# Kernel optimization log

Hardware: AMD Instinct MI355X
Metric: run time of the kernel (lower is better)

The kernel has to match this reference:

```python
import jax, jax.numpy as jnp
import numpy as np

N_NODES = 50000
N_EDGES = 400000
C_NODE = 128
C_EDGE = 256
# PyG: round(c_in + (c_out-c_in)*f)
H1, H2, H3 = 166, 192, 218


def setup_inputs() -> dict:
    key = jax.random.key(0)
    ks = jax.random.split(key, 20)
    x = jax.random.normal(ks[0], (N_NODES, C_NODE), dtype=jnp.float32)
    edge_index = jax.random.randint(ks[1], (2, N_EDGES), 0, N_NODES, dtype=jnp.int64)

    def glorot(k, fan_in, fan_out):
        s = jnp.sqrt(6.0 / (fan_in + fan_out)).astype(jnp.float32)
        return jax.random.uniform(k, (fan_in, fan_out), jnp.float32, -s, s)

    dims_e = [(C_NODE, H1), (H1, H2), (H2, H3), (H3, C_EDGE)]
    dims_n = [(C_NODE, C_NODE)] * 4
    inp = {"x": x, "edge_index": edge_index}
    for i, (fi, fo) in enumerate(dims_e, 1):
        inp[f"W{i}e"] = glorot(ks[1 + i], fi, fo)
        inp[f"b{i}e"] = jnp.zeros((fo,), jnp.float32)
    for i, (fi, fo) in enumerate(dims_n, 1):
        inp[f"W{i}n"] = glorot(ks[9 + i], fi, fo)
        inp[f"b{i}n"] = jnp.zeros((fo,), jnp.float32)
    return inp


def _gcn_norm(edge_index, n_nodes):
    # add self loops, then symmetric normalization (PyG gcn_norm, improved=False)
    loops = jnp.arange(n_nodes, dtype=edge_index.dtype)
    src = jnp.concatenate([edge_index[0], loops])
    dst = jnp.concatenate([edge_index[1], loops])
    deg = jax.ops.segment_sum(jnp.ones_like(dst, dtype=jnp.float32), dst, num_segments=n_nodes)
    dinv = jnp.where(deg > 0, jax.lax.rsqrt(deg), 0.0)
    norm = dinv[src] * dinv[dst]  # [E+N]
    return src, dst, norm


def _gcn_conv(h_in, W, b, src, dst, norm, n_nodes):
    h = h_in @ W                      # [N, C_out] dense transform first (PyG order)
    msg = h[src] * norm[:, None]      # gather + scale, [E+N, C_out]
    agg = jax.ops.segment_sum(msg, dst, num_segments=n_nodes)
    return agg + b


def _forward(x, edge_index, We, be, Wn, bn):
    n = x.shape[0]
    src, dst, norm = _gcn_norm(edge_index, n)
    e = x
    for i in range(4):
        e = _gcn_conv(e, We[i], be[i], src, dst, norm, n)
        e = jax.nn.relu(e) if i < 3 else jax.nn.sigmoid(e)
    v = x
    for i in range(4):
        v = _gcn_conv(v, Wn[i], bn[i], src, dst, norm, n)
        v = jax.nn.relu(v) if i < 3 else jax.nn.sigmoid(v)
    return e, v


def reference(x, edge_index, W1e, b1e, W2e, b2e, W3e, b3e, W4e, b4e,
              W1n, b1n, W2n, b2n, W3n, b3n, W4n, b4n):
    We = [W1e, W2e, W3e, W4e]
    be = [b1e, b2e, b3e, b4e]
    Wn = [W1n, W2n, W3n, W4n]
    bn = [b1n, b2n, b3n, b4n]
    return _forward(x, edge_index, We, be, Wn, bn)
```

## Files before the change

kernel.cpp:

```cpp
#include <hip/hip_runtime.h>
#include <hip/hip_bf16.h>
#include <cstdint>
#include <cstddef>

typedef __hip_bfloat16 bf16;
typedef __attribute__((ext_vector_type(8))) short bf16x8;
typedef __attribute__((ext_vector_type(4))) float f32x4;

#define NN 50000
#define NE 400000

struct PTab {
    const void* p[17];
    int n[17];
};

__device__ __forceinline__ float bf2f(unsigned short u) {
    return __uint_as_float(((unsigned)u) << 16);
}
__device__ __forceinline__ unsigned short f2bf(float f) {
    __hip_bfloat16 h = __float2bfloat16(f);
    return *reinterpret_cast<unsigned short*>(&h);
}
__device__ __forceinline__ float fin(float v) {
    return (v == v && v > -1e30f && v < 1e30f) ? v : 0.0f;
}
__device__ __forceinline__ float rd(const void* p, int i, int f) {
    return f ? ((const float*)p)[i] : bf2f(((const unsigned short*)p)[i]);
}

__device__ __forceinline__ void gl16(const void* g, void* l) {
    __builtin_amdgcn_global_load_lds(
        (const __attribute__((address_space(1))) unsigned int*)g,
        (__attribute__((address_space(3))) unsigned int*)l, 16, 0, 0);
}

__global__ void k_probe(PTab tab, const int* __restrict__ ei, int* __restrict__ flags) {
    __shared__ int zc, bc, sAny;
    for (int t = 0; t < 17; ++t) {
        if (threadIdx.x == 0) { zc = 0; bc = 0; }
        __syncthreads();
        int words = tab.n[t] >> 1;
        if (words > 256) words = 256;
        if ((int)threadIdx.x < words) {
            unsigned w = ((const unsigned*)tab.p[t])[threadIdx.x];
            if (w == 0u) atomicAdd(&zc, 1);
            else {
                int e = (w >> 7) & 0xFF;
                if (e >= 100 && e <= 140) atomicAdd(&bc, 1);
            }
        }
        __syncthreads();
        if (threadIdx.x == 0) {
            int nz = words - zc;
            flags[t] = (nz == 0 || 2 * bc >= nz) ? 0 : 1;
        }
        __syncthreads();
    }
    if (threadIdx.x == 0) sAny = 0;
    __syncthreads();
    int any = 0;
    for (int i = threadIdx.x; i < 2048; i += 256) any |= ei[2 * i + 1];
    if (any) sAny = 1;
    __syncthreads();
    if (threadIdx.x == 0) flags[17] = sAny;
}

struct WSeg {
    const void* src[8];
    unsigned short* wh[8];
    unsigned short* wl[8];
    int f[8], K[8], M[8], Kp[8];
    int b0[9];
};

__global__ void k_wsplitall(WSeg G, const int* __restrict__ flags) {
    int bid = blockIdx.x;
    int seg = 0;
    #pragma unroll
    for (int t = 1; t < 8; ++t) if (bid >= G.b0[t]) seg = t;
    int n = bid - G.b0[seg];
    int k = threadIdx.x;
    int Kp = G.Kp[seg];
    if (k >= Kp) return;
    float v = 0.0f;
    if (k < G.K[seg] && n < G.M[seg])
        v = fin(rd(G.src[seg], k * G.M[seg] + n, flags[G.f[seg]]));
    unsigned short hi = f2bf(v);
    unsigned short lo = f2bf(v - bf2f(hi));
    G.wh[seg][(size_t)n * Kp + k] = hi;
    G.wl[seg][(size_t)n * Kp + k] = lo;
}

struct MOff { int m[8]; int mp[8]; };

__global__ void k_biasall(PTab tab, const int* __restrict__ flags, MOff mo,
                          float* __restrict__ dst) {
    int l = blockIdx.x;
    int fidx = 2 + 2 * l;
    int M = tab.n[fidx];
    int i = threadIdx.x;
    if (i < mo.mp[l])
        dst[mo.m[l] + i] = (i < M) ? fin(rd(tab.p[fidx], i, flags[fidx])) : 0.0f;
}

__global__ void k_repack(const int* __restrict__ ei, const int* __restrict__ flags,
                         int* __restrict__ src, int* __restrict__ dst,
                         int* __restrict__ deg) {
    int e = blockIdx.x * blockDim.x + threadIdx.x;
    if (e >= NE) return;
    int s, d;
    if (flags[17]) { s = ei[e]; d = ei[NE + e]; }
    else           { s = ei[2 * e]; d = ei[2 * (NE + e)]; }
    s = min(max(s, 0), NN - 1);
    d = min(max(d, 0), NN - 1);
    src[e] = s;
    dst[e] = d;
    atomicAdd(&deg[d], 1);
}

__global__ void k_scan1(const int* __restrict__ deg, int* __restrict__ rowp,
                        int* __restrict__ part) {
    __shared__ int s[512];
    int tid = threadIdx.x, i = blockIdx.x * 512 + tid;
    int v = (i < NN) ? deg[i] : 0;
    s[tid] = v;
    __syncthreads();
    for (int off = 1; off < 512; off <<= 1) {
        int t = (tid >= off) ? s[tid - off] : 0;
        __syncthreads();
        s[tid] += t;
        __syncthreads();
    }
    if (i < NN) rowp[i] = s[tid] - v;
    if (tid == 511) part[blockIdx.x] = s[511];
}
__global__ void k_scan2(int* __restrict__ part, int nb) {
    __shared__ int s[128];
    int tid = threadIdx.x;
    int v = (tid < nb) ? part[tid] : 0;
    s[tid] = v;
    __syncthreads();
    for (int off = 1; off < 128; off <<= 1) {
        int t = (tid >= off) ? s[tid - off] : 0;
        __syncthreads();
        s[tid] += t;
        __syncthreads();
    }
    if (tid < nb) part[tid] = s[tid] - v;
}
__global__ void k_scan3(int* __restrict__ rowp, const int* __restrict__ part,
                        const int* __restrict__ deg, float* __restrict__ dinv) {
    int i = blockIdx.x * blockDim.x + threadIdx.x;
    if (i < NN) {
        rowp[i] += part[i >> 9];
        dinv[i] = rsqrtf((float)deg[i] + 1.0f);
    }
    if (i == 0) rowp[NN] = NE;
}

__global__ void k_fill(const int* __restrict__ src, const int* __restrict__ dst,
                       const int* __restrict__ rowp, int* __restrict__ cursor,
                       int* __restrict__ colv) {
    int e = blockIdx.x * blockDim.x + threadIdx.x;
    if (e >= NE) return;
    int d = dst[e];
    int p = atomicAdd(&cursor[d], 1);
    colv[rowp[d] + p] = src[e];
}

__global__ void k_xin(const void* __restrict__ x, const int* __restrict__ flags,
                      const float* __restrict__ dinv, unsigned short* __restrict__ xs) {
    int t = blockIdx.x * blockDim.x + threadIdx.x;
    if (t >= NN * 16) return;
    int i = t >> 4, c = (t & 15) * 8;
    float d = dinv[i];
    int f = flags[0];
    const float* xf = (const float*)x + (size_t)i * 128 + c;
    const unsigned short* xb = (const unsigned short*)x + (size_t)i * 128 + c;
    unsigned short o[8];
    #pragma unroll
    for (int j = 0; j < 8; ++j)
        o[j] = f2bf(fin(f ? xf[j] : bf2f(xb[j])) * d);
    *(uint4*)(xs + (size_t)i * 128 + c) = *(uint4*)o;
}

__launch_bounds__(256)
__global__ void k_gather(const unsigned short* __restrict__ in, int istride,
                         unsigned short* __restrict__ out, int ostride, int lanes,
                         const int* __restrict__ rowp, const int* __restrict__ colv,
                         const float* __restrict__ dinv) {
    const int node = blockIdx.x * 4 + (threadIdx.x >> 6);
    if (node >= NN) return;
    const int lane = threadIdx.x & 63;
    const int beg = rowp[node], end = rowp[node + 1];
    float a[8] = {0.f, 0.f, 0.f, 0.f, 0.f, 0.f, 0.f, 0.f};
    auto accq = [&](uint4 q) {
        unsigned v[4] = {q.x, q.y, q.z, q.w};
        #pragma unroll
        for (int t = 0; t < 4; ++t) {
            a[2 * t] += bf2f(v[t] & 0xFFFF); a[2 * t + 1] += bf2f(v[t] >> 16);
        }
    };
    if (lanes <= 16) {
        const int slot = lane >> 4;
        const int l8 = lane & 15;
        const bool on = l8 < lanes;
        const size_t off = (size_t)l8 * 8;
        if (slot == 0 && on)
            accq(*(const uint4*)(in + (size_t)node * istride + off));
        for (int j = beg + slot; j < end; j += 4) {
            const int s = colv[j];
            if (on) accq(*(const uint4*)(in + (size_t)s * istride + off));
        }
        #pragma unroll
        for (int t = 0; t < 8; ++t) {
            a[t] += __shfl_xor(a[t], 16);
            a[t] += __shfl_xor(a[t], 32);
        }
        if (lane < lanes) {
            float d = dinv[node];
            unsigned short o[8];
            #pragma unroll
            for (int t = 0; t < 8; ++t) o[t] = f2bf(a[t] * d);
            *(uint4*)(out + (size_t)node * ostride + (size_t)lane * 8) = *(uint4*)o;
        }
    } else {
        const bool on = lane < lanes;
        const size_t off = (size_t)lane * 8;
        if (on) accq(*(const uint4*)(in + (size_t)node * istride + off));
        int j = beg;
        for (; j + 8 <= end; j += 8) {
            int s0 = colv[j], s1 = colv[j + 1], s2 = colv[j + 2], s3 = colv[j + 3];
            int s4 = colv[j + 4], s5 = colv[j + 5], s6 = colv[j + 6], s7 = colv[j + 7];
            if (on) {
                uint4 q0 = *(const uint4*)(in + (size_t)s0 * istride + off);
                uint4 q1 = *(const uint4*)(in + (size_t)s1 * istride + off);
                uint4 q2 = *(const uint4*)(in + (size_t)s2 * istride + off);
                uint4 q3 = *(const uint4*)(in + (size_t)s3 * istride + off);
                uint4 q4 = *(const uint4*)(in + (size_t)s4 * istride + off);
                uint4 q5 = *(const uint4*)(in + (size_t)s5 * istride + off);
                uint4 q6 = *(const uint4*)(in + (size_t)s6 * istride + off);
                uint4 q7 = *(const uint4*)(in + (size_t)s7 * istride + off);
                accq(q0); accq(q1); accq(q2); accq(q3);
                accq(q4); accq(q5); accq(q6); accq(q7);
            }
        }
        if (j + 4 <= end) {
            int s0 = colv[j], s1 = colv[j + 1], s2 = colv[j + 2], s3 = colv[j + 3];
            if (on) {
                uint4 q0 = *(const uint4*)(in + (size_t)s0 * istride + off);
                uint4 q1 = *(const uint4*)(in + (size_t)s1 * istride + off);
                uint4 q2 = *(const uint4*)(in + (size_t)s2 * istride + off);
                uint4 q3 = *(const uint4*)(in + (size_t)s3 * istride + off);
                accq(q0); accq(q1); accq(q2); accq(q3);
            }
            j += 4;
        }
        if (j + 2 <= end) {
            int s0 = colv[j], s1 = colv[j + 1];
            if (on) {
                uint4 q0 = *(const uint4*)(in + (size_t)s0 * istride + off);
                uint4 q1 = *(const uint4*)(in + (size_t)s1 * istride + off);
                accq(q0); accq(q1);
            }
            j += 2;
        }
        if (j < end) {
            int s0 = colv[j];
            if (on) accq(*(const uint4*)(in + (size_t)s0 * istride + off));
        }
        if (on) {
            float d = dinv[node];
            unsigned short o[8];
            #pragma unroll
            for (int t = 0; t < 8; ++t) o[t] = f2bf(a[t] * d);
            *(uint4*)(out + (size_t)node * ostride + off) = *(uint4*)o;
        }
    }
}

struct GSide {
    const unsigned short* A;
    const unsigned short* Wh;
    const unsigned short* Wl;
    const float* bias;
    void* out;
    int Kp, ostride, M, OutW, act;
};

__launch_bounds__(256, 3)
__global__ void k_mgemm(GSide s0, GSide s1, int ySplit, int NY, int NB, int astride,
                        const float* __restrict__ dinv) {
    __shared__ __align__(16) unsigned char ldsraw[49152];
    auto sA  = reinterpret_cast<unsigned short (*)[128][32]>(ldsraw);
    auto sBh = reinterpret_cast<unsigned short (*)[128][32]>(ldsraw + 16384);
    auto sBl = reinterpret_cast<unsigned short (*)[128][32]>(ldsraw + 32768);

    const int tid = threadIdx.x;
    const int wave = tid >> 6, lane = tid & 63;
    const int wr = wave >> 1, wc = wave & 1;
    const int quad = lane >> 4, m16 = lane & 15;

    const int NBa = NB & ~7;
    const int swcut = NBa * NY;
    int b = blockIdx.x, x, yv;
    if (b < swcut) {
        x = (b / (8 * NY)) * 8 + (b & 7);
        yv = (b >> 3) % NY;
    } else {
        int r = b - swcut, rem = NB - NBa;
        x = rem ? (NBa + r % rem) : 0;
        yv = rem ? (r / rem) : 0;
    }

    GSide S; int ycol;
    if (yv < ySplit) { S = s0; ycol = yv; }
    else             { S = s1; ycol = yv - ySplit; }
    const int row0 = x * 128, col0 = ycol * 128;
    const int Kp = S.Kp;

    const int lr = lane >> 2;
    const int swz = ((lane >> 2) ^ (lane >> 4)) & 3;
    const int su = ((lane & 3) ^ swz) * 8;

    int ar1 = row0 + wave * 32 + lr;      if (ar1 >= NN) ar1 = NN - 1;
    int ar2 = row0 + wave * 32 + 16 + lr; if (ar2 >= NN) ar2 = NN - 1;
    const unsigned short* gA1 = S.A + (size_t)ar1 * astride + su;
    const unsigned short* gA2 = S.A + (size_t)ar2 * astride + su;
    const int br = col0 + wave * 32 + lr;
    const unsigned short* gBh1 = S.Wh + (size_t)br * Kp + su;
    const unsigned short* gBl1 = S.Wl + (size_t)br * Kp + su;

    f32x4 zz = {0.f, 0.f, 0.f, 0.f};
    f32x4 acc[4][4];
    #pragma unroll
    for (int i = 0; i < 4; ++i)
        #pragma unroll
        for (int j = 0; j < 4; ++j) acc[i][j] = zz;

    const int rs = (quad ^ ((m16 & 3) ^ ((m16 >> 2) & 3))) * 8;
    const int nk = Kp >> 5;

    auto stage = [&](int bb, int k0) {
        gl16(gA1 + k0,            &sA[bb][wave * 32][0]);
        gl16(gA2 + k0,            &sA[bb][wave * 32 + 16][0]);
        gl16(gBh1 + k0,           &sBh[bb][wave * 32][0]);
        gl16(gBh1 + 16 * Kp + k0, &sBh[bb][wave * 32 + 16][0]);
        gl16(gBl1 + k0,           &sBl[bb][wave * 32][0]);
        gl16(gBl1 + 16 * Kp + k0, &sBl[bb][wave * 32 + 16][0]);
    };

    stage(0, 0);
    __syncthreads();
    int cur = 0;
    for (int ks = 0; ks < nk; ++ks) {
        if (ks + 1 < nk) stage(cur ^ 1, (ks + 1) * 32);
        bf16x8 fa[4], fh[4], fl[4];
        #pragma unroll
        for (int i = 0; i < 4; ++i) {
            fa[i] = *(const bf16x8*)&sA[cur][wr * 64 + i * 16 + m16][rs];
            fh[i] = *(const bf16x8*)&sBh[cur][wc * 64 + i * 16 + m16][rs];
            fl[i] = *(const bf16x8*)&sBl[cur][wc * 64 + i * 16 + m16][rs];
        }
        #pragma unroll
        for (int i = 0; i < 4; ++i)
            #pragma unroll
            for (int j = 0; j < 4; ++j) {
                acc[i][j] = __builtin_amdgcn_mfma_f32_16x16x32_bf16(fa[i], fh[j], acc[i][j], 0, 0, 0);
                acc[i][j] = __builtin_amdgcn_mfma_f32_16x16x32_bf16(fa[i], fl[j], acc[i][j], 0, 0, 0);
            }
        __syncthreads();
        cur ^= 1;
    }

    float* eps = (float*)(ldsraw + (size_t)wave * 4352);
    #pragma unroll
    for (int i = 0; i < 4; ++i) {
        #pragma unroll
        for (int j = 0; j < 4; ++j) {
            int col = col0 + wc * 64 + j * 16 + m16;
            float bcol = (col < S.M) ? S.bias[col] : 0.0f;
            #pragma unroll
            for (int r = 0; r < 4; ++r) {
                float v = acc[i][j][r] + bcol;
                if (S.act) v = (col < S.M) ? 1.0f / (1.0f + expf(-v)) : 0.0f;
                else       v = (col < S.M) ? fmaxf(v, 0.0f) : 0.0f;
                eps[(quad * 4 + r) * 68 + j * 16 + m16] = v;
            }
        }
        asm volatile("s_waitcnt lgkmcnt(0)" ::: "memory");
        __builtin_amdgcn_sched_barrier(0);
        #pragma unroll
        for (int it = 0; it < 4; ++it) {
            int lr2 = it * 4 + (lane >> 4);
            int c4 = (lane & 15) * 4;
            float4 w = *(float4*)&eps[lr2 * 68 + c4];
            int grow = row0 + wr * 64 + i * 16 + lr2;
            int gcol = col0 + wc * 64 + c4;
            if (grow < NN && gcol < S.OutW) {
                if (S.act) {
                    *(float4*)((float*)S.out + (size_t)grow * S.ostride + gcol) = w;
                } else {
                    float d = dinv[grow];
                    unsigned o0 = f2bf(w.x * d) | ((unsigned)f2bf(w.y * d) << 16);
                    unsigned o1 = f2bf(w.z * d) | ((unsigned)f2bf(w.w * d) << 16);
                    uint2 u; u.x = o0; u.y = o1;
                    *(uint2*)((unsigned short*)S.out + (size_t)grow * S.ostride + gcol) = u;
                }
            }
        }
        asm volatile("s_waitcnt lgkmcnt(0)" ::: "memory");
        __builtin_amdgcn_sched_barrier(0);
    }
}

__global__ void k_sentinel(float* __restrict__ out, int n) {
    int i = blockIdx.x * blockDim.x + threadIdx.x;
    if (i < n) out[i] = 4.0f;
}

extern "C" void kernel_launch(void* const* d_in, const int* in_sizes, int n_in,
                              void* d_out, int out_size, void* d_ws, size_t ws_size,
                              hipStream_t stream) {
    const int* ei = (const int*)d_in[1];
    float* out_e = (float*)d_out;
    float* out_v = out_e + (size_t)NN * 256;

    const int wsz[16] = {128 * 166, 166, 166 * 192, 192, 192 * 218, 218, 218 * 256, 256,
                         128 * 128, 128, 128 * 128, 128, 128 * 128, 128, 128 * 128, 128};
    PTab tab;
    tab.p[0] = d_in[0]; tab.n[0] = NN * 128;
    for (int t = 0; t < 16; ++t) { tab.p[t + 1] = d_in[2 + t]; tab.n[t + 1] = wsz[t]; }

    const int KpW[8] = {128, 192, 192, 224, 0, 128, 128, 128};
    const int MpW[8] = {384, 256, 256, 256, 0, 128, 128, 128};

    char* wsb = (char*)d_ws;
    size_t o = 0;
    auto align = [](size_t v) { return (v + 255) & ~(size_t)255; };
    int*   flags  = (int*)(wsb + o);  o = align(o + 128);
    int*   colv   = (int*)(wsb + o);  o = align(o + (size_t)NE * 4);
    int*   deg    = (int*)(wsb + o);  o = align(o + (size_t)NN * 4);
    int*   cursor = (int*)(wsb + o);  o = align(o + (size_t)NN * 4);
    int*   rowp   = (int*)(wsb + o);  o = align(o + (size_t)(NN + 1) * 4);
    int*   part   = (int*)(wsb + o);  o = align(o + 512);
    float* dinv   = (float*)(wsb + o); o = align(o + (size_t)NN * 4);
    unsigned short* wh[8]; unsigned short* wl[8];
    for (int l = 0; l < 8; ++l) {
        size_t wel = (size_t)MpW[l] * KpW[l];
        wh[l] = (unsigned short*)(wsb + o); o = align(o + wel * 2);
        wl[l] = (unsigned short*)(wsb + o); o = align(o + wel * 2);
    }
    float* ball = (float*)(wsb + o); o = align(o + 1376 * 4);
    unsigned short* bufA = (unsigned short*)(wsb + o); o = align(o + (size_t)NN * 352 * 2);
    unsigned short* bufB = (unsigned short*)(wsb + o); o = align(o + (size_t)NN * 352 * 2);
    int* src32 = (int*)bufB;
    int* dst32 = src32 + NE;
    if (o > ws_size) {
        k_sentinel<<<(out_size + 255) / 256, 256, 0, stream>>>(out_e, out_size);
        return;
    }

    MOff mo;
    const int moff[8] = {0, 296, 616, 968, 168, 488, 840, 1224};
    const int mpad[8] = {168, 192, 224, 256, 128, 128, 128, 128};
    for (int l = 0; l < 8; ++l) { mo.m[l] = moff[l]; mo.mp[l] = mpad[l]; }

    const int EB = (NE + 255) / 256;
    const int NB512 = (NN + 511) / 512;
    const int GX = (NN + 127) / 128;
    const int GN = (NN + 3) / 4;

    k_probe<<<1, 256, 0, stream>>>(tab, ei, flags);

    {
        WSeg G;
        const void* srcs[8] = {d_in[2], d_in[10], d_in[4], d_in[12],
                               d_in[6], d_in[14], d_in[8], d_in[16]};
        unsigned short* whp[8] = {wh[0], wh[0] + 168 * 128, wh[1], wh[5],
                                  wh[2], wh[6], wh[3], wh[7]};
        unsigned short* wlp[8] = {wl[0], wl[0] + 168 * 128, wl[1], wl[5],
                                  wl[2], wl[6], wl[3], wl[7]};
        const int fs[8]  = {1, 9, 3, 11, 5, 13, 7, 15};
        const int Ks[8]  = {128, 128, 166, 128, 192, 128, 218, 128};
        const int Ms[8]  = {166, 128, 192, 128, 218, 128, 256, 128};
        const int Kps[8] = {128, 128, 192, 128, 192, 128, 224, 128};
        const int rows[8] = {168, 216, 256, 128, 256, 128, 256, 128};
        int acc = 0;
        for (int s = 0; s < 8; ++s) {
            G.src[s] = srcs[s]; G.wh[s] = whp[s]; G.wl[s] = wlp[s];
            G.f[s] = fs[s]; G.K[s] = Ks[s]; G.M[s] = Ms[s]; G.Kp[s] = Kps[s];
            G.b0[s] = acc; acc += rows[s];
        }
        G.b0[8] = acc;
        k_wsplitall<<<acc, 256, 0, stream>>>(G, flags);
    }
    k_biasall<<<8, 256, 0, stream>>>(tab, flags, mo, ball);

    hipMemsetAsync(deg, 0, (size_t)NN * 4, stream);
    hipMemsetAsync(cursor, 0, (size_t)NN * 4, stream);
    k_repack<<<EB, 256, 0, stream>>>(ei, flags, src32, dst32, deg);
    k_scan1<<<NB512, 512, 0, stream>>>(deg, rowp, part);
    k_scan2<<<1, 128, 0, stream>>>(part, NB512);
    k_scan3<<<(NN + 255) / 256, 256, 0, stream>>>(rowp, part, deg, dinv);
    k_fill<<<EB, 256, 0, stream>>>(src32, dst32, rowp, cursor, colv);

    k_xin<<<(NN * 16 + 255) / 256, 256, 0, stream>>>(d_in[0], flags, dinv, bufA);
    k_gather<<<GN, 256, 0, stream>>>(bufA, 128, bufB, 128, 16, rowp, colv, dinv);

    {
        GSide s0 = {bufB, wh[0], wl[0], ball, bufA, 128, 296, 296, 296, 0};
        k_mgemm<<<GX * 3, 256, 0, stream>>>(s0, s0, 3, 3, GX, 128, dinv);
    }
    k_gather<<<GN, 256, 0, stream>>>(bufA, 296, bufB, 296, 37, rowp, colv, dinv);

    {
        GSide s0 = {bufB, wh[1], wl[1], ball + 616, bufA, 192, 320, 192, 192, 0};
        GSide s1 = {bufB + 168, wh[5], wl[5], ball + 488, bufA + 192, 128, 320, 128, 128, 0};
        s0.bias = ball + 296;
        k_mgemm<<<GX * 3, 256, 0, stream>>>(s0, s1, 2, 3, GX, 296, dinv);
    }
    k_gather<<<GN, 256, 0, stream>>>(bufA, 320, bufB, 320, 40, rowp, colv, dinv);

    {
        GSide s0 = {bufB, wh[2], wl[2], ball + 616, bufA, 192, 352, 218, 224, 0};
        GSide s1 = {bufB + 192, wh[6], wl[6], ball + 840, bufA + 224, 128, 352, 128, 128, 0};
        k_mgemm<<<GX * 3, 256, 0, stream>>>(s0, s1, 2, 3, GX, 320, dinv);
    }
    k_gather<<<GN, 256, 0, stream>>>(bufA, 352, bufB, 352, 44, rowp, colv, dinv);

    {
        GSide s0 = {bufB, wh[3], wl[3], ball + 968, out_e, 224, 256, 256, 256, 1};
        GSide s1 = {bufB + 224, wh[7], wl[7], ball + 1224, out_v, 128, 128, 128, 128, 1};
        k_mgemm<<<GX * 3, 256, 0, stream>>>(s0, s1, 2, 3, GX, 352, dinv);
    }
}
```

Before: 515.4 us.

## Prefetch two K-tiles ahead in GEMM with vmcnt waits; shrink gather unroll

The MFMA GEMM main loop now issues loads for the next two K-tiles. It waits with explicit s_waitcnt vmcnt counts and raw s_barrier instead of __syncthreads, so global-to-LDS copies overlap the MFMA work of the current tile. The gather kernel's 8/4/2-way unrolled neighbour loop is replaced by a simple 2-way loop, which cuts code size and register pressure but leaves fewer loads in flight. The bias pointer setup is also tidied. The hand-counted vmcnt(6) is correct only if each stage call issues exactly six loads.

```diff
diff --git a/kernel.cpp b/kernel.cpp
--- a/kernel.cpp
+++ b/kernel.cpp
@@ -230,41 +230,13 @@
         const size_t off = (size_t)lane * 8;
         if (on) accq(*(const uint4*)(in + (size_t)node * istride + off));
         int j = beg;
-        for (; j + 8 <= end; j += 8) {
-            int s0 = colv[j], s1 = colv[j + 1], s2 = colv[j + 2], s3 = colv[j + 3];
-            int s4 = colv[j + 4], s5 = colv[j + 5], s6 = colv[j + 6], s7 = colv[j + 7];
-            if (on) {
-                uint4 q0 = *(const uint4*)(in + (size_t)s0 * istride + off);
-                uint4 q1 = *(const uint4*)(in + (size_t)s1 * istride + off);
-                uint4 q2 = *(const uint4*)(in + (size_t)s2 * istride + off);
-                uint4 q3 = *(const uint4*)(in + (size_t)s3 * istride + off);
-                uint4 q4 = *(const uint4*)(in + (size_t)s4 * istride + off);
-                uint4 q5 = *(const uint4*)(in + (size_t)s5 * istride + off);
-                uint4 q6 = *(const uint4*)(in + (size_t)s6 * istride + off);
-                uint4 q7 = *(const uint4*)(in + (size_t)s7 * istride + off);
-                accq(q0); accq(q1); accq(q2); accq(q3);
-                accq(q4); accq(q5); accq(q6); accq(q7);
-            }
-        }
-        if (j + 4 <= end) {
-            int s0 = colv[j], s1 = colv[j + 1], s2 = colv[j + 2], s3 = colv[j + 3];
-            if (on) {
-                uint4 q0 = *(const uint4*)(in + (size_t)s0 * istride + off);
-                uint4 q1 = *(const uint4*)(in + (size_t)s1 * istride + off);
-                uint4 q2 = *(const uint4*)(in + (size_t)s2 * istride + off);
-                uint4 q3 = *(const uint4*)(in + (size_t)s3 * istride + off);
-                accq(q0); accq(q1); accq(q2); accq(q3);
-            }
-            j += 4;
-        }
-        if (j + 2 <= end) {
+        for (; j + 1 < end; j += 2) {
             int s0 = colv[j], s1 = colv[j + 1];
             if (on) {
                 uint4 q0 = *(const uint4*)(in + (size_t)s0 * istride + off);
                 uint4 q1 = *(const uint4*)(in + (size_t)s1 * istride + off);
                 accq(q0); accq(q1);
             }
-            j += 2;
         }
         if (j < end) {
             int s0 = colv[j];
@@ -352,10 +324,13 @@
     };
 
     stage(0, 0);
-    __syncthreads();
-    int cur = 0;
+    if (nk > 1) stage(1, 32);
+
     for (int ks = 0; ks < nk; ++ks) {
-        if (ks + 1 < nk) stage(cur ^ 1, (ks + 1) * 32);
+        const int cur = ks & 1;
+        if (ks + 1 < nk) asm volatile("s_waitcnt vmcnt(6)" ::: "memory");
+        else             asm volatile("s_waitcnt vmcnt(0)" ::: "memory");
+        __builtin_amdgcn_s_barrier();
         bf16x8 fa[4], fh[4], fl[4];
         #pragma unroll
         for (int i = 0; i < 4; ++i) {
@@ -363,6 +338,10 @@
             fh[i] = *(const bf16x8*)&sBh[cur][wc * 64 + i * 16 + m16][rs];
             fl[i] = *(const bf16x8*)&sBl[cur][wc * 64 + i * 16 + m16][rs];
         }
+        asm volatile("s_waitcnt lgkmcnt(0)" ::: "memory");
+        __builtin_amdgcn_sched_barrier(0);
+        __builtin_amdgcn_s_barrier();
+        if (ks + 2 < nk) stage(cur, (ks + 2) * 32);
         #pragma unroll
         for (int i = 0; i < 4; ++i)
             #pragma unroll
@@ -370,8 +349,6 @@
                 acc[i][j] = __builtin_amdgcn_mfma_f32_16x16x32_bf16(fa[i], fh[j], acc[i][j], 0, 0, 0);
                 acc[i][j] = __builtin_amdgcn_mfma_f32_16x16x32_bf16(fa[i], fl[j], acc[i][j], 0, 0, 0);
             }
-        __syncthreads();
-        cur ^= 1;
     }
 
     float* eps = (float*)(ldsraw + (size_t)wave * 4352);
@@ -516,9 +493,8 @@
     k_gather<<<GN, 256, 0, stream>>>(bufA, 296, bufB, 296, 37, rowp, colv, dinv);
 
     {
-        GSide s0 = {bufB, wh[1], wl[1], ball + 616, bufA, 192, 320, 192, 192, 0};
+        GSide s0 = {bufB, wh[1], wl[1], ball + 296, bufA, 192, 320, 192, 192, 0};
         GSide s1 = {bufB + 168, wh[5], wl[5], ball + 488, bufA + 192, 128, 320, 128, 128, 0};
-        s0.bias = ball + 296;
         k_mgemm<<<GX * 3, 256, 0, stream>>>(s0, s1, 2, 3, GX, 296, dinv);
     }
     k_gather<<<GN, 256, 0, stream>>>(bufA, 320, bufB, 320, 40, rowp, colv, dinv);
```

After: 508.6 us. About the same (-1.3%).
